# Kernel tuning notes

Hardware: AMD Instinct MI355X
Metric: run time of the kernel (lower is better)

The kernel has to match this reference:

```python
import jax, jax.numpy as jnp
import numpy as np

INPUT_NDIMS = 1024
HIDDEN = 512
LATENT = 50
BATCH = 16384

def setup_inputs() -> dict:
    key = jax.random.key(0)
    ks = jax.random.split(key, 12)
    s = 0.02
    x = jax.random.uniform(ks[0], (BATCH, INPUT_NDIMS), dtype=jnp.float32)
    u = 0.01 + 0.98 * jax.random.uniform(ks[1], (BATCH, LATENT), dtype=jnp.float32)
    W1 = s * jax.random.normal(ks[2], (HIDDEN, INPUT_NDIMS), dtype=jnp.float32)
    b1 = jnp.zeros((HIDDEN,), jnp.float32)
    Wa = s * jax.random.normal(ks[3], (LATENT, HIDDEN), dtype=jnp.float32)
    ba = jnp.zeros((LATENT,), jnp.float32)
    Wb = s * jax.random.normal(ks[4], (LATENT, HIDDEN), dtype=jnp.float32)
    bb = jnp.zeros((LATENT,), jnp.float32)
    W2 = s * jax.random.normal(ks[5], (HIDDEN, LATENT), dtype=jnp.float32)
    b2 = jnp.zeros((HIDDEN,), jnp.float32)
    W3 = s * jax.random.normal(ks[6], (INPUT_NDIMS, HIDDEN), dtype=jnp.float32)
    b3 = jnp.zeros((INPUT_NDIMS,), jnp.float32)
    return dict(x=x, u=u, W1=W1, b1=b1, Wa=Wa, ba=ba, Wb=Wb, bb=bb, W2=W2, b2=b2, W3=W3, b3=b3)

def _stick_segments(v):
    # pi[:, k] = v[:, k] * prod_{j<k} (1 - v[:, j])  -- single O(K) cumprod pass
    cp = jnp.cumprod(1.0 - v, axis=1)                       # inclusive cumprod
    excl = jnp.concatenate([jnp.ones_like(cp[:, :1]), cp[:, :-1]], axis=1)
    return v * excl

def reference(x, u, W1, b1, Wa, ba, Wb, bb, W2, b2, W3, b3):
    # encoder: MLP -> positive Kumaraswamy params alpha (param1), beta (param2)
    h = jax.nn.relu(x @ W1.T + b1)                           # [B, H]
    alpha = jax.nn.softplus(h @ Wa.T + ba) + 1e-4            # [B, K]
    beta = jax.nn.softplus(h @ Wb.T + bb) + 1e-4             # [B, K]
    # Kumaraswamy reparameterized sample: v = (1 - u^(1/beta))^(1/alpha)
    v = jnp.power(1.0 - jnp.power(u, 1.0 / beta), 1.0 / alpha)
    # set_v_K_to_one: force last stick fraction to 1 so segments sum to 1
    v = v.at[:, -1].set(1.0)
    pi = _stick_segments(v)                                  # [B, K], rows sum to 1
    # decoder: MLP with sigmoid output
    h2 = jax.nn.relu(pi @ W2.T + b2)                         # [B, H]
    recon = jax.nn.sigmoid(h2 @ W3.T + b3)                   # [B, D]
    return recon, alpha, beta
```

## Files before the change

kernel.cpp:

```cpp
#include <hip/hip_runtime.h>
#include <hip/hip_bf16.h>

typedef __hip_bfloat16 bf16_t;
typedef __attribute__((ext_vector_type(4))) float f32x4;
typedef __attribute__((ext_vector_type(8))) __bf16 bf16x8;
typedef __attribute__((ext_vector_type(8))) short s16x8;
typedef __attribute__((ext_vector_type(4))) unsigned short u16x4;

#define BATCH 16384
#define NDIM  1024
#define HID   512
#define LAT   50

#define LOG2E 1.44269504088896340736f
#define RLOG2E 0.69314718055994530942f

__device__ __forceinline__ float ex2(float x) { return __builtin_amdgcn_exp2f(x); }
__device__ __forceinline__ float lg2(float x) { return __builtin_amdgcn_logf(x); }
__device__ __forceinline__ float rcp(float x) { return __builtin_amdgcn_rcpf(x); }

__device__ inline unsigned short f2b_u(float f) {
  union { bf16_t b; unsigned short u; } cv; cv.b = __float2bfloat16(f); return cv.u;
}

__device__ __forceinline__ void gload16(const void* src, void* dst_lds) {
  __builtin_amdgcn_global_load_lds(
      reinterpret_cast<const __attribute__((address_space(1))) void*>(
          reinterpret_cast<unsigned long long>(src)),
      reinterpret_cast<__attribute__((address_space(3))) void*>(
          static_cast<unsigned>(reinterpret_cast<unsigned long long>(dst_lds))),
      16, 0, 0);
}

__global__ void prep_w_kernel(const float* __restrict__ W1, const float* __restrict__ W3,
                              const float* __restrict__ Wa, const float* __restrict__ Wb,
                              const float* __restrict__ W2, const float* __restrict__ ba,
                              const float* __restrict__ bb,
                              bf16_t* __restrict__ w1, bf16_t* __restrict__ w3,
                              bf16_t* __restrict__ wab, bf16_t* __restrict__ w2p,
                              float* __restrict__ bab)
{
  const int W1U  = (HID * NDIM) / 4;
  const int W3U  = (NDIM * HID) / 4;
  const int WABN = 128 * HID;
  const int W2PN = HID * 64;
  const int TOT  = W1U + W3U + WABN + W2PN + 128;
  for (int i = blockIdx.x * blockDim.x + threadIdx.x; i < TOT;
       i += gridDim.x * blockDim.x) {
    int j = i;
    if (j < W1U) {
      const f32x4 v = ((const f32x4*)W1)[j];
      u16x4 o; o[0]=f2b_u(v[0]); o[1]=f2b_u(v[1]); o[2]=f2b_u(v[2]); o[3]=f2b_u(v[3]);
      ((u16x4*)w1)[j] = o; continue;
    }
    j -= W1U;
    if (j < W3U) {
      const f32x4 v = ((const f32x4*)W3)[j];
      u16x4 o; o[0]=f2b_u(v[0]); o[1]=f2b_u(v[1]); o[2]=f2b_u(v[2]); o[3]=f2b_u(v[3]);
      ((u16x4*)w3)[j] = o; continue;
    }
    j -= W3U;
    if (j < WABN) {
      const int n = j >> 9, k = j & 511;
      float v = (n < 50) ? Wa[n * 512 + k] : ((n < 100) ? Wb[(n - 50) * 512 + k] : 0.f);
      wab[j] = __float2bfloat16(v); continue;
    }
    j -= WABN;
    if (j < W2PN) {
      const int n = j >> 6, k = j & 63;
      w2p[j] = __float2bfloat16(k < 50 ? W2[n * 50 + k] : 0.f); continue;
    }
    j -= W2PN;
    bab[j] = (j < 50) ? ba[j] : ((j < 100) ? bb[j - 50] : 0.f);
  }
}

template<int A_F32, int EPI, int MT>
__global__ __launch_bounds__(256, 4)
void gemm_kernel(const void* __restrict__ Av, const bf16_t* __restrict__ B,
                 const float* __restrict__ bias, void* __restrict__ out0,
                 float* __restrict__ out_a, float* __restrict__ out_b,
                 int M, int N, int K)
{
  constexpr int MI = MT / 32;
  __shared__ char lds[MT * 128 + 16384];
  char* lA = lds;
  char* lB = lds + MT * 128;

  const int tid  = threadIdx.x;
  const int swzid = ((blockIdx.x & 7) * (gridDim.x >> 3)) + (blockIdx.x >> 3);
  const int nblocks = N >> 7;
  const int bn   = swzid % nblocks;
  const int bm   = swzid / nblocks;
  const int wid  = tid >> 6;
  const int lane = tid & 63;
  const int l15  = lane & 15;
  const int l4   = lane >> 4;
  const int wm   = (wid >> 1) * (MT / 2);
  const int wn   = (wid & 1) << 6;
  const int uw   = __builtin_amdgcn_readfirstlane(wid);

  f32x4 acc[MI][4] = {};

  for (int k0 = 0; k0 < K; k0 += 64) {
    #pragma unroll
    for (int i = 0; i < 4; ++i) {
      const int c  = (i * 4 + uw) * 64 + lane;
      const int r  = c >> 3;
      const int sp = c & 7;
      const int sl = sp ^ (r & 7);
      gload16(B + (size_t)(bn * 128 + r) * K + k0 + sl * 8,
              lB + (i * 4 + uw) * 1024);
    }
    if (A_F32) {
      const float* A = (const float*)Av;
      #pragma unroll
      for (int i = 0; i < MI; ++i) {
        const int c  = i * 256 + tid;
        const int r  = c >> 3;
        const int sl = c & 7;
        const int sp = sl ^ (r & 7);
        const float* s = A + (size_t)(bm * MT + r) * K + k0 + sl * 8;
        const f32x4 v0 = *(const f32x4*)s;
        const f32x4 v1 = *(const f32x4*)(s + 4);
        union { s16x8 v; unsigned short us[8]; } o;
        o.us[0]=f2b_u(v0[0]); o.us[1]=f2b_u(v0[1]); o.us[2]=f2b_u(v0[2]); o.us[3]=f2b_u(v0[3]);
        o.us[4]=f2b_u(v1[0]); o.us[5]=f2b_u(v1[1]); o.us[6]=f2b_u(v1[2]); o.us[7]=f2b_u(v1[3]);
        *(s16x8*)(lA + r * 128 + sp * 16) = o.v;
      }
    } else {
      const bf16_t* A = (const bf16_t*)Av;
      #pragma unroll
      for (int i = 0; i < MI; ++i) {
        const int c  = (i * 4 + uw) * 64 + lane;
        const int r  = c >> 3;
        const int sp = c & 7;
        const int sl = sp ^ (r & 7);
        gload16(A + (size_t)(bm * MT + r) * K + k0 + sl * 8,
                lA + (i * 4 + uw) * 1024);
      }
    }
    __syncthreads();

    #pragma unroll
    for (int h = 0; h < 2; ++h) {
      bf16x8 af[MI], bfr[4];
      #pragma unroll
      for (int mi = 0; mi < MI; ++mi) {
        const int row = wm + mi * 16 + l15;
        const int sp  = (h * 4 + l4) ^ (row & 7);
        af[mi] = *(const bf16x8*)(lA + row * 128 + sp * 16);
      }
      #pragma unroll
      for (int ni = 0; ni < 4; ++ni) {
        const int row = wn + ni * 16 + l15;
        const int sp  = (h * 4 + l4) ^ (row & 7);
        bfr[ni] = *(const bf16x8*)(lB + row * 128 + sp * 16);
      }
      #pragma unroll
      for (int mi = 0; mi < MI; ++mi)
        #pragma unroll
        for (int ni = 0; ni < 4; ++ni)
          acc[mi][ni] = __builtin_amdgcn_mfma_f32_16x16x32_bf16(
              af[mi], bfr[ni], acc[mi][ni], 0, 0, 0);
    }
    __syncthreads();
  }

  #pragma unroll
  for (int ni = 0; ni < 4; ++ni) {
    const int n  = bn * 128 + wn + ni * 16 + l15;
    const float bv = bias[n];
    #pragma unroll
    for (int mi = 0; mi < MI; ++mi) {
      #pragma unroll
      for (int r = 0; r < 4; ++r) {
        const int m  = bm * MT + wm + mi * 16 + l4 * 4 + r;
        const float t = acc[mi][ni][r] + bv;
        if (EPI == 2) {
          if (n < 100) {
            const float y =
                (t > 20.f ? t : lg2(1.f + ex2(t * LOG2E)) * RLOG2E) + 1e-4f;
            if (n < 50) out_a[(size_t)m * 50 + n] = y;
            else        out_b[(size_t)m * 50 + (n - 50)] = y;
          }
        } else if (EPI == 0) {
          ((bf16_t*)out0)[(size_t)m * N + n] = __float2bfloat16(fmaxf(t, 0.f));
        } else {
          ((float*)out0)[(size_t)m * N + n] = rcp(1.f + ex2(-t * LOG2E));
        }
      }
    }
  }
}

__global__ void stick_kernel(const float* __restrict__ u,
                             const float* __restrict__ alpha,
                             const float* __restrict__ beta,
                             bf16_t* __restrict__ pi)
{
  const int gw   = (blockIdx.x * blockDim.x + threadIdx.x) >> 6;
  const int lane = threadIdx.x & 63;
  if (gw >= BATCH) return;
  const size_t row = (size_t)gw;

  float v = 1.f, t = 1.f;
  if (lane < 49) {
    const float a  = alpha[row * 50 + lane];
    const float b  = beta[row * 50 + lane];
    const float uu = u[row * 50 + lane];
    const float tb = ex2(lg2(uu) * rcp(b));
    v = ex2(lg2(1.f - tb) * rcp(a));
    t = 1.f - v;
  }
  float p = t;
  #pragma unroll
  for (int d = 1; d < 64; d <<= 1) {
    const float o = __shfl_up(p, d, 64);
    if (lane >= d) p *= o;
  }
  float e = __shfl_up(p, 1, 64);
  if (lane == 0) e = 1.f;
  pi[row * 64 + lane] = __float2bfloat16(lane < 50 ? v * e : 0.f);
}

extern "C" void kernel_launch(void* const* d_in, const int* in_sizes, int n_in,
                              void* d_out, int out_size, void* d_ws, size_t ws_size,
                              hipStream_t stream)
{
  const float* x  = (const float*)d_in[0];
  const float* u  = (const float*)d_in[1];
  const float* W1 = (const float*)d_in[2];
  const float* b1 = (const float*)d_in[3];
  const float* Wa = (const float*)d_in[4];
  const float* ba = (const float*)d_in[5];
  const float* Wb = (const float*)d_in[6];
  const float* bb = (const float*)d_in[7];
  const float* W2 = (const float*)d_in[8];
  const float* b2 = (const float*)d_in[9];
  const float* W3 = (const float*)d_in[10];
  const float* b3 = (const float*)d_in[11];

  float* recon  = (float*)d_out;
  float* oalpha = recon + (size_t)BATCH * NDIM;
  float* obeta  = oalpha + (size_t)BATCH * LAT;

  char* ws = (char*)d_ws;
  bf16_t* h   = (bf16_t*)(ws);
  bf16_t* h2  = (bf16_t*)(ws + 16777216);
  bf16_t* pi  = (bf16_t*)(ws + 33554432);
  bf16_t* w1  = (bf16_t*)(ws + 35651584);
  bf16_t* w3  = (bf16_t*)(ws + 36700160);
  bf16_t* wab = (bf16_t*)(ws + 37748736);
  bf16_t* w2p = (bf16_t*)(ws + 37879808);
  float*  bab = (float*)(ws + 37945344);

  prep_w_kernel<<<512, 256, 0, stream>>>(W1, W3, Wa, Wb, W2, ba, bb,
                                         w1, w3, wab, w2p, bab);
  gemm_kernel<1, 0, 64><<<1024, 256, 0, stream>>>(
      x, w1, b1, (void*)h, nullptr, nullptr, BATCH, HID, NDIM);
  gemm_kernel<0, 2, 64><<<256, 256, 0, stream>>>(
      h, wab, bab, nullptr, oalpha, obeta, BATCH, 128, HID);
  stick_kernel<<<4096, 256, 0, stream>>>(u, oalpha, obeta, pi);
  gemm_kernel<0, 0, 64><<<1024, 256, 0, stream>>>(
      pi, w2p, b2, (void*)h2, nullptr, nullptr, BATCH, HID, 64);
  gemm_kernel<0, 1, 128><<<1024, 256, 0, stream>>>(
      h2, w3, b3, (void*)recon, nullptr, nullptr, BATCH, NDIM, HID);
}
```

Measured before the change: 87.30 us.

## Double-buffer LDS in GEMM kernel to overlap global loads with MFMA

Restructures the GEMM main loop into a software pipeline. The next K-tile is loaded into a second LDS buffer (for fp32 A, into registers and converted after compute) while MFMAs run on the current tile, which leaves one barrier per iteration. It also switches the first GEMM to 128-row tiles with half as many blocks. Shared memory use doubles and launch-bound occupancy drops to 2-3 blocks per CU, and the register-staged fp32 path adds register pressure.

```diff
diff --git a/kernel.cpp b/kernel.cpp
--- a/kernel.cpp
+++ b/kernel.cpp
@@ -75,17 +75,16 @@
   }
 }
 
-template<int A_F32, int EPI, int MT>
-__global__ __launch_bounds__(256, 4)
+template<int A_F32, int EPI, int MT, int DB>
+__global__ __launch_bounds__(256, DB ? (MT == 128 ? 2 : 3) : 4)
 void gemm_kernel(const void* __restrict__ Av, const bf16_t* __restrict__ B,
                  const float* __restrict__ bias, void* __restrict__ out0,
                  float* __restrict__ out_a, float* __restrict__ out_b,
                  int M, int N, int K)
 {
-  constexpr int MI = MT / 32;
-  __shared__ char lds[MT * 128 + 16384];
-  char* lA = lds;
-  char* lB = lds + MT * 128;
+  constexpr int MI  = MT / 32;
+  constexpr int BUF = MT * 128 + 16384;
+  __shared__ char lds[(DB ? 2 : 1) * BUF];
 
   const int tid  = threadIdx.x;
   const int swzid = ((blockIdx.x & 7) * (gridDim.x >> 3)) + (blockIdx.x >> 3);
@@ -101,8 +100,10 @@
   const int uw   = __builtin_amdgcn_readfirstlane(wid);
 
   f32x4 acc[MI][4] = {};
-
-  for (int k0 = 0; k0 < K; k0 += 64) {
+  f32x4 areg[2 * MI];
+
+  auto stage_B = [&](char* buf, int k0) {
+    char* lB = buf + MT * 128;
     #pragma unroll
     for (int i = 0; i < 4; ++i) {
       const int c  = (i * 4 + uw) * 64 + lane;
@@ -112,36 +113,48 @@
       gload16(B + (size_t)(bn * 128 + r) * K + k0 + sl * 8,
               lB + (i * 4 + uw) * 1024);
     }
-    if (A_F32) {
-      const float* A = (const float*)Av;
-      #pragma unroll
-      for (int i = 0; i < MI; ++i) {
-        const int c  = i * 256 + tid;
-        const int r  = c >> 3;
-        const int sl = c & 7;
-        const int sp = sl ^ (r & 7);
-        const float* s = A + (size_t)(bm * MT + r) * K + k0 + sl * 8;
-        const f32x4 v0 = *(const f32x4*)s;
-        const f32x4 v1 = *(const f32x4*)(s + 4);
-        union { s16x8 v; unsigned short us[8]; } o;
-        o.us[0]=f2b_u(v0[0]); o.us[1]=f2b_u(v0[1]); o.us[2]=f2b_u(v0[2]); o.us[3]=f2b_u(v0[3]);
-        o.us[4]=f2b_u(v1[0]); o.us[5]=f2b_u(v1[1]); o.us[6]=f2b_u(v1[2]); o.us[7]=f2b_u(v1[3]);
-        *(s16x8*)(lA + r * 128 + sp * 16) = o.v;
-      }
-    } else {
-      const bf16_t* A = (const bf16_t*)Av;
-      #pragma unroll
-      for (int i = 0; i < MI; ++i) {
-        const int c  = (i * 4 + uw) * 64 + lane;
-        const int r  = c >> 3;
-        const int sp = c & 7;
-        const int sl = sp ^ (r & 7);
-        gload16(A + (size_t)(bm * MT + r) * K + k0 + sl * 8,
-                lA + (i * 4 + uw) * 1024);
-      }
-    }
-    __syncthreads();
-
+  };
+  auto stage_A_bf16 = [&](char* buf, int k0) {
+    const bf16_t* A = (const bf16_t*)Av;
+    #pragma unroll
+    for (int i = 0; i < MI; ++i) {
+      const int c  = (i * 4 + uw) * 64 + lane;
+      const int r  = c >> 3;
+      const int sp = c & 7;
+      const int sl = sp ^ (r & 7);
+      gload16(A + (size_t)(bm * MT + r) * K + k0 + sl * 8,
+              buf + (i * 4 + uw) * 1024);
+    }
+  };
+  auto load_A_f32 = [&](int k0) {
+    const float* A = (const float*)Av;
+    #pragma unroll
+    for (int i = 0; i < MI; ++i) {
+      const int c  = i * 256 + tid;
+      const int r  = c >> 3;
+      const int sl = c & 7;
+      const float* s = A + (size_t)(bm * MT + r) * K + k0 + sl * 8;
+      areg[2 * i]     = *(const f32x4*)s;
+      areg[2 * i + 1] = *(const f32x4*)(s + 4);
+    }
+  };
+  auto write_A_f32 = [&](char* buf) {
+    #pragma unroll
+    for (int i = 0; i < MI; ++i) {
+      const int c  = i * 256 + tid;
+      const int r  = c >> 3;
+      const int sl = c & 7;
+      const int sp = sl ^ (r & 7);
+      union { s16x8 v; unsigned short us[8]; } o;
+      const f32x4 v0 = areg[2 * i], v1 = areg[2 * i + 1];
+      o.us[0]=f2b_u(v0[0]); o.us[1]=f2b_u(v0[1]); o.us[2]=f2b_u(v0[2]); o.us[3]=f2b_u(v0[3]);
+      o.us[4]=f2b_u(v1[0]); o.us[5]=f2b_u(v1[1]); o.us[6]=f2b_u(v1[2]); o.us[7]=f2b_u(v1[3]);
+      *(s16x8*)(buf + r * 128 + sp * 16) = o.v;
+    }
+  };
+  auto compute = [&](const char* buf) {
+    const char* lA = buf;
+    const char* lB = buf + MT * 128;
     #pragma unroll
     for (int h = 0; h < 2; ++h) {
       bf16x8 af[MI], bfr[4];
@@ -164,8 +177,27 @@
           acc[mi][ni] = __builtin_amdgcn_mfma_f32_16x16x32_bf16(
               af[mi], bfr[ni], acc[mi][ni], 0, 0, 0);
     }
+  };
+
+  const int nt = K >> 6;
+  if (A_F32) { load_A_f32(0); write_A_f32(lds); }
+  else       { stage_A_bf16(lds, 0); }
+  stage_B(lds, 0);
+  __syncthreads();
+
+  int cur = 0;
+  for (int t = 0; t < nt - 1; ++t) {
+    char* nbuf = lds + (DB ? (cur ^ 1) * BUF : 0);
+    const int k0n = (t + 1) << 6;
+    if (A_F32) load_A_f32(k0n);
+    else       stage_A_bf16(nbuf, k0n);
+    stage_B(nbuf, k0n);
+    compute(lds + cur * BUF);
+    if (A_F32) write_A_f32(nbuf);
     __syncthreads();
-  }
+    cur ^= 1;
+  }
+  compute(lds + cur * BUF);
 
   #pragma unroll
   for (int ni = 0; ni < 4; ++ni) {
@@ -257,13 +289,13 @@
 
   prep_w_kernel<<<512, 256, 0, stream>>>(W1, W3, Wa, Wb, W2, ba, bb,
                                          w1, w3, wab, w2p, bab);
-  gemm_kernel<1, 0, 64><<<1024, 256, 0, stream>>>(
+  gemm_kernel<1, 0, 128, 1><<<512, 256, 0, stream>>>(
       x, w1, b1, (void*)h, nullptr, nullptr, BATCH, HID, NDIM);
-  gemm_kernel<0, 2, 64><<<256, 256, 0, stream>>>(
+  gemm_kernel<0, 2, 64, 1><<<256, 256, 0, stream>>>(
       h, wab, bab, nullptr, oalpha, obeta, BATCH, 128, HID);
   stick_kernel<<<4096, 256, 0, stream>>>(u, oalpha, obeta, pi);
-  gemm_kernel<0, 0, 64><<<1024, 256, 0, stream>>>(
+  gemm_kernel<0, 0, 64, 0><<<1024, 256, 0, stream>>>(
       pi, w2p, b2, (void*)h2, nullptr, nullptr, BATCH, HID, 64);
-  gemm_kernel<0, 1, 128><<<1024, 256, 0, stream>>>(
+  gemm_kernel<0, 1, 128, 1><<<1024, 256, 0, stream>>>(
       h2, w3, b3, (void*)recon, nullptr, nullptr, BATCH, NDIM, HID);
 }
```

New measurement: 86.07 us. About the same (-1.4%).
